# Kernel tuning notes

Measured on AMD Instinct MI355X. Metric: run time of the kernel, lower is better.

The kernel has to match this reference:

```python
import jax, jax.numpy as jnp
import numpy as np

ANCHORS = jnp.array([[1.3221, 1.73145], [3.19275, 4.00944], [5.05587, 8.09892],
                     [9.47112, 4.84053], [11.2364, 10.0071]], dtype=jnp.float32)
NUM_ANCHORS = 5
NUM_CLASSES = 20
MAX_BOXES = 50
NOOBJECT_SCALE = 1.0
OBJECT_SCALE = 5.0
COORD_SCALE = 1.0
CLASS_SCALE = 1.0
SIL_THRESH = 0.6


def iou_cwh(b1, b2):
    # boxes as (cx, cy, w, h); matches repo bbox_ious(x1y1x2y2=False)
    x1, y1, w1, h1 = b1[..., 0], b1[..., 1], b1[..., 2], b1[..., 3]
    x2, y2, w2, h2 = b2[..., 0], b2[..., 1], b2[..., 2], b2[..., 3]
    uw = jnp.maximum(x1 + w1 * 0.5, x2 + w2 * 0.5) - jnp.minimum(x1 - w1 * 0.5, x2 - w2 * 0.5)
    uh = jnp.maximum(y1 + h1 * 0.5, y2 + h2 * 0.5) - jnp.minimum(y1 - h1 * 0.5, y2 - h2 * 0.5)
    cw = w1 + w2 - uw
    ch = h1 + h2 - uh
    inter = jnp.where((cw <= 0) | (ch <= 0), 0.0, cw * ch)
    return inter / (w1 * h1 + w2 * h2 - inter)


def setup_inputs() -> dict:
    key = jax.random.key(0)
    k1, k2, k3, k4 = jax.random.split(key, 4)
    nB = 64
    output = jax.random.normal(k1, (nB, NUM_ANCHORS * (5 + NUM_CLASSES), 38, 38), dtype=jnp.float32)
    # target layout per box: (class, x, y, w, h), all normalized; x>0 marks a valid box
    cls_col = jax.random.randint(k2, (nB, MAX_BOXES, 1), 0, NUM_CLASSES).astype(jnp.float32)
    xy = jax.random.uniform(k3, (nB, MAX_BOXES, 2), minval=0.05, maxval=0.95)
    wh = jax.random.uniform(k4, (nB, MAX_BOXES, 2), minval=0.02, maxval=0.3)
    target = jnp.concatenate([cls_col, xy, wh], axis=-1).reshape(nB, MAX_BOXES * 5)
    return {"output": output, "target": target}


def region_loss(output, target):
    nB = output.shape[0]
    nA, nC = NUM_ANCHORS, NUM_CLASSES
    nH, nW = output.shape[2], output.shape[3]
    out = output.reshape(nB, nA, 5 + nC, nH, nW)
    x = jax.nn.sigmoid(out[:, :, 0])
    y = jax.nn.sigmoid(out[:, :, 1])
    w = out[:, :, 2]
    h = out[:, :, 3]
    conf = jax.nn.sigmoid(out[:, :, 4])
    # [nB,nA,nC,nH,nW] -> [nB*nA*nH*nW, nC] (matches torch transpose/view order)
    cls_logits = jnp.transpose(out[:, :, 5:], (0, 1, 3, 4, 2)).reshape(-1, nC)

    sg = jax.lax.stop_gradient
    aw, ah = ANCHORS[:, 0], ANCHORS[:, 1]
    grid_x = jnp.arange(nW, dtype=jnp.float32)[None, None, None, :]
    grid_y = jnp.arange(nH, dtype=jnp.float32)[None, None, :, None]
    px = sg(x) + grid_x
    py = sg(y) + grid_y
    pw = jnp.exp(sg(w)) * aw[None, :, None, None]
    ph = jnp.exp(sg(h)) * ah[None, :, None, None]
    pred_boxes = jnp.stack([px, py, pw, ph], axis=-1)  # [nB,nA,nH,nW,4]

    # ---- build_targets (vectorized) ----
    tgt = sg(target).reshape(nB, MAX_BOXES, 5)
    gcls = tgt[:, :, 0]
    gx = tgt[:, :, 1] * nW
    gy = tgt[:, :, 2] * nH
    gw = tgt[:, :, 3] * nW
    gh = tgt[:, :, 4] * nH
    # loop breaks at first x==0 -> cumulative validity
    valid = jnp.cumprod((tgt[:, :, 1] != 0).astype(jnp.int32), axis=1).astype(bool)

    # silence conf_mask where any-GT IoU > thresh
    pb_flat = pred_boxes.reshape(nB, nA * nH * nW, 4)
    gt_boxes = jnp.stack([gx, gy, gw, gh], axis=-1)  # [nB,50,4]
    ious = iou_cwh(pb_flat[:, :, None, :], gt_boxes[:, None, :, :])  # [nB,nAnc,50]
    ious = jnp.where(valid[:, None, :], ious, 0.0)
    max_iou = jnp.max(ious, axis=2)
    conf_mask = jnp.where(max_iou > SIL_THRESH, 0.0, NOOBJECT_SCALE).reshape(nB, nA, nH, nW)

    # seen < 12800 defaults
    shp = (nB, nA, nH, nW)
    coord_mask = jnp.ones(shp, jnp.float32)
    tx = jnp.full(shp, 0.5, jnp.float32)
    ty = jnp.full(shp, 0.5, jnp.float32)
    tw = jnp.zeros(shp, jnp.float32)
    th = jnp.zeros(shp, jnp.float32)
    tconf = jnp.zeros(shp, jnp.float32)
    tcls = jnp.zeros(shp, jnp.float32)
    cls_mask = jnp.zeros(shp, jnp.float32)

    # best anchor per GT by (0,0,w,h) IoU; argmax keeps first max like the strict '>' loop
    zA = jnp.zeros_like(aw)
    anchor_boxes = jnp.stack([zA, zA, aw, ah], axis=-1)  # [nA,4]
    zg = jnp.zeros_like(gw)
    gt_wh = jnp.stack([zg, zg, gw, gh], axis=-1)  # [nB,50,4]
    a_iou = iou_cwh(gt_wh[:, :, None, :], anchor_boxes[None, None, :, :])  # [nB,50,nA]
    best_n = jnp.argmax(a_iou, axis=2)  # [nB,50]

    gi = jnp.clip(gx.astype(jnp.int32), 0, nW - 1)
    gj = jnp.clip(gy.astype(jnp.int32), 0, nH - 1)
    aw_b = aw[best_n]
    ah_b = ah[best_n]
    tx_v = gx - gi.astype(jnp.float32)
    ty_v = gy - gj.astype(jnp.float32)
    tw_v = jnp.log(gw / aw_b)
    th_v = jnp.log(gh / ah_b)
    b_ix = jnp.arange(nB)
    pred_at = pred_boxes[b_ix[:, None], best_n, gj, gi]  # [nB,50,4]
    iou_gt = iou_cwh(gt_boxes, pred_at)  # [nB,50]

    def step(carry, t):
        cm, clm, tx_, ty_, tw_, th_, tcf, tcl = carry
        bsel = jnp.where(valid[:, t], b_ix, nB)  # out-of-bounds -> dropped
        n, j, i = best_n[:, t], gj[:, t], gi[:, t]
        st = lambda a, v: a.at[bsel, n, j, i].set(v, mode='drop')
        cm = st(cm, jnp.full((nB,), OBJECT_SCALE, jnp.float32))
        clm = st(clm, jnp.ones((nB,), jnp.float32))
        tx_ = st(tx_, tx_v[:, t])
        ty_ = st(ty_, ty_v[:, t])
        tw_ = st(tw_, tw_v[:, t])
        th_ = st(th_, th_v[:, t])
        tcf = st(tcf, iou_gt[:, t])
        tcl = st(tcl, gcls[:, t])
        return (cm, clm, tx_, ty_, tw_, th_, tcf, tcl), None

    init = (conf_mask, cls_mask, tx, ty, tw, th, tconf, tcls)
    (conf_mask, cls_mask, tx, ty, tw, th, tconf, tcls), _ = jax.lax.scan(
        step, init, jnp.arange(MAX_BOXES))

    # ---- losses ----
    cmf = jnp.sqrt(conf_mask)
    loss_x = COORD_SCALE * jnp.sum((x * coord_mask - tx * coord_mask) ** 2) / 2.0
    loss_y = COORD_SCALE * jnp.sum((y * coord_mask - ty * coord_mask) ** 2) / 2.0
    loss_w = COORD_SCALE * jnp.sum((w * coord_mask - tw * coord_mask) ** 2) / 2.0
    loss_h = COORD_SCALE * jnp.sum((h * coord_mask - th * coord_mask) ** 2) / 2.0
    loss_conf = jnp.sum((conf * cmf - tconf * cmf) ** 2) / 2.0
    logp = jax.nn.log_softmax(cls_logits, axis=-1)
    labels = tcls.reshape(-1).astype(jnp.int32)
    ce = -jnp.take_along_axis(logp, labels[:, None], axis=1)[:, 0]
    loss_cls = CLASS_SCALE * jnp.sum(ce * cls_mask.reshape(-1))
    return loss_x + loss_y + loss_w + loss_h + loss_conf + loss_cls


def reference(output, target):
    return region_loss(output, target)
```

## Files before the change

### kernel.cpp

```cpp
#include <hip/hip_runtime.h>
#include <math.h>

#define NA 5
#define NC 20
#define NH 38
#define NW 38
#define MAX_BOXES 50
#define SPAT (NH * NW)
#define CELLS_PER_B (NA * SPAT)
#define TPB 256
#define CELLS_PER_T 2
#define CPB (TPB * CELLS_PER_T)
#define GX ((CELLS_PER_B + CPB - 1) / CPB)
#define OBJECT_SCALE 5.0f
#define NOOBJECT_SCALE 1.0f

__constant__ float c_aw[NA]  = {1.3221f, 3.19275f, 5.05587f, 9.47112f, 11.2364f};
__constant__ float c_ah[NA]  = {1.73145f, 4.00944f, 8.09892f, 4.84053f, 10.0071f};
__constant__ float c_iaw[NA] = {1.f/1.3221f, 1.f/3.19275f, 1.f/5.05587f, 1.f/9.47112f, 1.f/11.2364f};
__constant__ float c_iah[NA] = {1.f/1.73145f, 1.f/4.00944f, 1.f/8.09892f, 1.f/4.84053f, 1.f/10.0071f};

__device__ __forceinline__ float fexp(float v) { return __expf(v); }
__device__ __forceinline__ float flog(float v) { return __logf(v); }
__device__ __forceinline__ float frcp(float v) { return __builtin_amdgcn_rcpf(v); }
__device__ __forceinline__ float fsig(float v) { return frcp(1.f + __expf(-v)); }

__device__ __forceinline__ float iou_fast(float x1, float y1, float w1, float h1,
                                          float x2, float y2, float w2, float h2) {
  float uw = fmaxf(x1 + w1 * 0.5f, x2 + w2 * 0.5f) - fminf(x1 - w1 * 0.5f, x2 - w2 * 0.5f);
  float uh = fmaxf(y1 + h1 * 0.5f, y2 + h2 * 0.5f) - fminf(y1 - h1 * 0.5f, y2 - h2 * 0.5f);
  float cw = w1 + w2 - uw;
  float ch = h1 + h2 - uh;
  float inter = (cw <= 0.f || ch <= 0.f) ? 0.f : cw * ch;
  return inter * frcp(w1 * h1 + w2 * h2 - inter);
}

__device__ __forceinline__ float iou_wh_exact(float w1, float h1, float w2, float h2) {
  float uw = fmaxf(w1 * 0.5f, w2 * 0.5f) - fminf(-w1 * 0.5f, -w2 * 0.5f);
  float uh = fmaxf(h1 * 0.5f, h2 * 0.5f) - fminf(-h1 * 0.5f, -h2 * 0.5f);
  float cw = w1 + w2 - uw;
  float ch = h1 + h2 - uh;
  float inter = (cw <= 0.f || ch <= 0.f) ? 0.f : cw * ch;
  return inter / (w1 * h1 + w2 * h2 - inter);
}

__global__ __launch_bounds__(TPB) void region_loss_kernel(
    const float* __restrict__ out, const float* __restrict__ target,
    float* __restrict__ partials) {
  const int b = blockIdx.y;
  const int s0 = blockIdx.x * CPB;
  const int tid = threadIdx.x;

  __shared__ float4 sb_lo[MAX_BOXES];
  __shared__ float  sb_ag[MAX_BOXES];
  __shared__ int s_wcnt;
  __shared__ int s_wcell[MAX_BOXES];
  __shared__ float s_wdata[MAX_BOXES][6];
  __shared__ float s_red[TPB / 64];

  int sC[CELLS_PER_T];
  bool ok[CELLS_PER_T];
  const float* basep[CELLS_PER_T];
  float v0[CELLS_PER_T], v1[CELLS_PER_T], v2[CELLS_PER_T], v3[CELLS_PER_T], v4[CELLS_PER_T];
  float fi[CELLS_PER_T], fj[CELLS_PER_T], paw[CELLS_PER_T], pah[CELLS_PER_T];
#pragma unroll
  for (int q = 0; q < CELLS_PER_T; ++q) {
    int s = s0 + q * TPB + tid;
    ok[q] = (s < CELLS_PER_B);
    int sc = ok[q] ? s : 0;
    sC[q] = ok[q] ? s : -1;
    unsigned a = (unsigned)sc / SPAT;
    unsigned r = (unsigned)sc - a * SPAT;
    unsigned j = r / NW, i = r - j * NW;
    fi[q] = (float)i; fj[q] = (float)j;
    paw[q] = c_aw[a]; pah[q] = c_ah[a];
    const float* bp = out + ((size_t)(b * NA + a) * 25) * SPAT + r;
    basep[q] = bp;
    v0[q] = bp[0];
    v1[q] = bp[SPAT];
    v2[q] = bp[2 * SPAT];
    v3[q] = bp[3 * SPAT];
    v4[q] = bp[4 * SPAT];
  }

  if (tid == TPB - 1) s_wcnt = 0;
  __syncthreads();

  if (tid < 64) {
    int t = tid;
    float cls = 0.f, x = 0.f, y = 0.f, w = 0.f, h = 0.f;
    if (t < MAX_BOXES) {
      const float* tg = target + (size_t)(b * MAX_BOXES + t) * 5;
      cls = tg[0]; x = tg[1]; y = tg[2]; w = tg[3]; h = tg[4];
    }
    unsigned long long nz = __ballot(t < MAX_BOXES && x != 0.f);
    unsigned long long low = (t < 63) ? ((1ull << (t + 1)) - 1ull) : ~0ull;
    bool valid = (t < MAX_BOXES) && ((nz & low) == low);

    float gx = x * NW, gy = y * NH, gw = w * NW, gh = h * NH;

    int best = 0; float bestiou = -1.f;
#pragma unroll
    for (int a2 = 0; a2 < NA; ++a2) {
      float aiou = iou_wh_exact(gw, gh, c_aw[a2], c_ah[a2]);
      if (aiou > bestiou) { bestiou = aiou; best = a2; }
    }
    int gi = min(max((int)gx, 0), NW - 1);
    int gj = min(max((int)gy, 0), NH - 1);

    const float* pb = out + ((size_t)(b * NA + best) * 25) * SPAT + gj * NW + gi;
    float px = fsig(pb[0]) + (float)gi;
    float py = fsig(pb[SPAT]) + (float)gj;
    float pw2 = fexp(pb[2 * SPAT]) * c_aw[best];
    float ph2 = fexp(pb[3 * SPAT]) * c_ah[best];
    float iou_gt = iou_fast(gx, gy, gw, gh, px, py, pw2, ph2);

    int cell = best * SPAT + gj * NW + gi;
    unsigned long long vm = __ballot(valid);
    bool winner = valid;
    for (int tp = 0; tp < MAX_BOXES; ++tp) {
      int c2 = __shfl(cell, tp);
      if (tp > t && ((vm >> tp) & 1ull) && c2 == cell) winner = false;
    }

    if (t < MAX_BOXES) {
      if (valid) {
        sb_lo[t] = make_float4(gx - gw * 0.5f, gx + gw * 0.5f,
                               gy - gh * 0.5f, gy + gh * 0.5f);
        sb_ag[t] = 0.375f * (gw * gh);
      } else {
        sb_lo[t] = make_float4(1e30f, 1e30f, 1e30f, 1e30f);
        sb_ag[t] = 0.f;
      }
      if (winner && cell >= s0 && cell < s0 + CPB) {
        int k = atomicAdd(&s_wcnt, 1);
        s_wcell[k] = cell;
        s_wdata[k][0] = gx - (float)gi;
        s_wdata[k][1] = gy - (float)gj;
        s_wdata[k][2] = flog(gw * c_iaw[best]);
        s_wdata[k][3] = flog(gh * c_iah[best]);
        s_wdata[k][4] = iou_gt;
        s_wdata[k][5] = cls;
      }
    }
  }
  __syncthreads();

  float xs[CELLS_PER_T], ys[CELLS_PER_T], cs[CELLS_PER_T];
  float plx[CELLS_PER_T], phx[CELLS_PER_T], ply[CELLS_PER_T], phy[CELLS_PER_T];
  float ap[CELLS_PER_T], msc[CELLS_PER_T];
#pragma unroll
  for (int q = 0; q < CELLS_PER_T; ++q) {
    xs[q] = fsig(v0[q]);
    ys[q] = fsig(v1[q]);
    cs[q] = fsig(v4[q]);
    float pw = fexp(v2[q]) * paw[q], ph = fexp(v3[q]) * pah[q];
    float px = xs[q] + fi[q], py = ys[q] + fj[q];
    plx[q] = px - pw * 0.5f; phx[q] = px + pw * 0.5f;
    ply[q] = py - ph * 0.5f; phy[q] = py + ph * 0.5f;
    ap[q] = 0.375f * (pw * ph);
    msc[q] = -1e30f;
  }

#pragma unroll
  for (int c0 = 0; c0 < MAX_BOXES; c0 += 10) {
    float4 bl[10]; float bag[10];
#pragma unroll
    for (int u = 0; u < 10; ++u) { bl[u] = sb_lo[c0 + u]; bag[u] = sb_ag[c0 + u]; }
#pragma unroll
    for (int u = 0; u < 10; ++u) {
#pragma unroll
      for (int q = 0; q < CELLS_PER_T; ++q) {
        float cw = fminf(phx[q], bl[u].y) - fmaxf(plx[q], bl[u].x);
        float ch = fminf(phy[q], bl[u].w) - fmaxf(ply[q], bl[u].z);
        cw = fmaxf(cw, 0.f);
        msc[q] = fmaxf(msc[q], fmaf(cw, ch, -bag[u]));
      }
    }
  }

  int cnt = s_wcnt;
  float acc = 0.f;
#pragma unroll
  for (int q = 0; q < CELLS_PER_T; ++q) {
    if (!ok[q]) continue;
    float cmask = (msc[q] > ap[q]) ? 0.f : NOOBJECT_SCALE;
    float tx = 0.5f, ty = 0.5f, tw = 0.f, th = 0.f, tconf = 0.f, clsloss = 0.f;
    for (int k = 0; k < cnt; ++k) {
      if (s_wcell[k] == sC[q]) {
        cmask = OBJECT_SCALE;
        tx = s_wdata[k][0]; ty = s_wdata[k][1];
        tw = s_wdata[k][2]; th = s_wdata[k][3];
        tconf = s_wdata[k][4];
        int label = (int)s_wdata[k][5];
        const float* cb = basep[q] + 5 * SPAT;
        float m = -1e30f, lv = 0.f;
        for (int c = 0; c < NC; ++c) {
          float vv = cb[c * SPAT];
          if (c == label) lv = vv;
          m = fmaxf(m, vv);
        }
        float ssum = 0.f;
        for (int c = 0; c < NC; ++c) ssum += fexp(cb[c * SPAT] - m);
        clsloss = (m + flog(ssum)) - lv;
      }
    }
    float dx = xs[q] - tx, dy = ys[q] - ty, dw = v2[q] - tw, dh = v3[q] - th;
    float dc = cs[q] - tconf;
    acc += 0.5f * (dx * dx + dy * dy + dw * dw + dh * dh + cmask * (dc * dc)) + clsloss;
  }

  for (int o = 32; o > 0; o >>= 1) acc += __shfl_down(acc, o, 64);
  int wid = tid >> 6, lane = tid & 63;
  if (lane == 0) s_red[wid] = acc;
  __syncthreads();
  if (tid == 0) {
    float v = 0.f;
#pragma unroll
    for (int wdx = 0; wdx < TPB / 64; ++wdx) v += s_red[wdx];
    partials[blockIdx.y * GX + blockIdx.x] = v;
  }
}

__global__ __launch_bounds__(256) void reduce_kernel(
    const float* __restrict__ partials, int n, float* __restrict__ outv) {
  float acc = 0.f;
  for (int i = threadIdx.x; i < n; i += 256) acc += partials[i];
  for (int o = 32; o > 0; o >>= 1) acc += __shfl_down(acc, o, 64);
  __shared__ float s_red[4];
  int wid = threadIdx.x >> 6, lane = threadIdx.x & 63;
  if (lane == 0) s_red[wid] = acc;
  __syncthreads();
  if (threadIdx.x == 0) outv[0] = s_red[0] + s_red[1] + s_red[2] + s_red[3];
}

extern "C" void kernel_launch(void* const* d_in, const int* in_sizes, int n_in,
                              void* d_out, int out_size, void* d_ws, size_t ws_size,
                              hipStream_t stream) {
  const float* out = (const float*)d_in[0];
  const float* target = (const float*)d_in[1];
  int nB = in_sizes[0] / (NA * (5 + NC) * SPAT);
  float* partials = (float*)d_ws;
  hipLaunchKernelGGL(region_loss_kernel, dim3(GX, nB), dim3(TPB), 0, stream,
                     out, target, partials);
  hipLaunchKernelGGL(reduce_kernel, dim3(1), dim3(256), 0, stream,
                     partials, GX * nB, (float*)d_out);
}
```

Before: 118.4 us.

## Split winner-cell correction into prep kernel and simplify main loss pass

Moves the per-target processing (anchor matching, winner detection, box prep) into a separate per-batch prep kernel. That kernel writes the box list and a per-batch correction delta, the object-cell loss minus the default no-object loss. The main kernel then computes only the uniform default loss per cell, dropping the per-cell scan over winners, the softmax branch and the per-block target recomputation. The cost is an extra launch and global round trip for the boxes, and it relies on the winner cell's default term being subtracted exactly.

Result: faster. 104.7 us (-11.5%).

```diff
diff --git a/kernel.cpp b/kernel.cpp
--- a/kernel.cpp
+++ b/kernel.cpp
@@ -44,8 +44,108 @@
   return inter / (w1 * h1 + w2 * h2 - inter);
 }
 
-__global__ __launch_bounds__(TPB) void region_loss_kernel(
+__global__ __launch_bounds__(64) void prep_kernel(
     const float* __restrict__ out, const float* __restrict__ target,
+    float4* __restrict__ boxes, float* __restrict__ delta) {
+  const int b = blockIdx.x;
+  const int t = threadIdx.x;
+  __shared__ float4 sb_lo[MAX_BOXES];
+  __shared__ float  sb_ag[MAX_BOXES];
+
+  float cls = 0.f, x = 0.f, y = 0.f, w = 0.f, h = 0.f;
+  if (t < MAX_BOXES) {
+    const float* tg = target + (size_t)(b * MAX_BOXES + t) * 5;
+    cls = tg[0]; x = tg[1]; y = tg[2]; w = tg[3]; h = tg[4];
+  }
+  unsigned long long nz = __ballot(t < MAX_BOXES && x != 0.f);
+  unsigned long long low = (t < 63) ? ((1ull << (t + 1)) - 1ull) : ~0ull;
+  bool valid = (t < MAX_BOXES) && ((nz & low) == low);
+
+  float gx = x * NW, gy = y * NH, gw = w * NW, gh = h * NH;
+
+  int best = 0; float bestiou = -1.f;
+#pragma unroll
+  for (int a2 = 0; a2 < NA; ++a2) {
+    float aiou = iou_wh_exact(gw, gh, c_aw[a2], c_ah[a2]);
+    if (aiou > bestiou) { bestiou = aiou; best = a2; }
+  }
+  int gi = min(max((int)gx, 0), NW - 1);
+  int gj = min(max((int)gy, 0), NH - 1);
+  int cell = best * SPAT + gj * NW + gi;
+
+  unsigned long long vm = __ballot(valid);
+  bool winner = valid;
+  for (int tp = 0; tp < MAX_BOXES; ++tp) {
+    int c2 = __shfl(cell, tp);
+    if (tp > t && ((vm >> tp) & 1ull) && c2 == cell) winner = false;
+  }
+
+  float4 lo; float ag;
+  if (valid) {
+    lo = make_float4(gx - gw * 0.5f, gx + gw * 0.5f, gy - gh * 0.5f, gy + gh * 0.5f);
+    ag = 0.375f * (gw * gh);
+  } else {
+    lo = make_float4(1e30f, 1e30f, 1e30f, 1e30f);
+    ag = 0.f;
+  }
+  if (t < MAX_BOXES) {
+    boxes[(size_t)(b * MAX_BOXES + t) * 2]     = lo;
+    boxes[(size_t)(b * MAX_BOXES + t) * 2 + 1] = make_float4(ag, 0.f, 0.f, 0.f);
+    sb_lo[t] = lo;
+    sb_ag[t] = ag;
+  }
+  __syncthreads();
+
+  float d = 0.f;
+  if (winner) {
+    const float* bp = out + ((size_t)(b * NA + best) * 25) * SPAT + gj * NW + gi;
+    float v0 = bp[0], v1 = bp[SPAT], v2 = bp[2 * SPAT], v3 = bp[3 * SPAT], v4 = bp[4 * SPAT];
+    float xs = fsig(v0), ys = fsig(v1), cs = fsig(v4);
+    float pw = fexp(v2) * c_aw[best], ph = fexp(v3) * c_ah[best];
+    float px = xs + (float)gi, py = ys + (float)gj;
+    float plx = px - pw * 0.5f, phx = px + pw * 0.5f;
+    float ply = py - ph * 0.5f, phy = py + ph * 0.5f;
+    float ap = 0.375f * (pw * ph);
+
+    float msc = -1e30f;
+    for (int t2 = 0; t2 < MAX_BOXES; ++t2) {
+      float4 l2 = sb_lo[t2];
+      float cw = fminf(phx, l2.y) - fmaxf(plx, l2.x);
+      float ch = fminf(phy, l2.w) - fmaxf(ply, l2.z);
+      cw = fmaxf(cw, 0.f);
+      msc = fmaxf(msc, fmaf(cw, ch, -sb_ag[t2]));
+    }
+    float cmask_def = (msc > ap) ? 0.f : NOOBJECT_SCALE;
+    float xd = xs - 0.5f, yd = ys - 0.5f;
+    float D = 0.5f * (xd * xd + yd * yd + v2 * v2 + v3 * v3 + cmask_def * (cs * cs));
+
+    float txv = gx - (float)gi, tyv = gy - (float)gj;
+    float twv = flog(gw * c_iaw[best]), thv = flog(gh * c_iah[best]);
+    float tconf = iou_fast(gx, gy, gw, gh, px, py, pw, ph);
+    float dx = xs - txv, dy = ys - tyv, dwv = v2 - twv, dhv = v3 - thv, dc = cs - tconf;
+
+    int label = (int)cls;
+    const float* cb = bp + 5 * SPAT;
+    float m = -1e30f, lv = 0.f;
+    for (int c = 0; c < NC; ++c) {
+      float vv = cb[c * SPAT];
+      if (c == label) lv = vv;
+      m = fmaxf(m, vv);
+    }
+    float ssum = 0.f;
+    for (int c = 0; c < NC; ++c) ssum += fexp(cb[c * SPAT] - m);
+    float ce = (m + flog(ssum)) - lv;
+
+    float W = 0.5f * (dx * dx + dy * dy + dwv * dwv + dhv * dhv +
+                      OBJECT_SCALE * (dc * dc)) + ce;
+    d = W - D;
+  }
+  for (int o = 32; o > 0; o >>= 1) d += __shfl_down(d, o, 64);
+  if (t == 0) delta[b] = d;
+}
+
+__global__ __launch_bounds__(TPB) void main_kernel(
+    const float* __restrict__ out, const float4* __restrict__ boxes,
     float* __restrict__ partials) {
   const int b = blockIdx.y;
   const int s0 = blockIdx.x * CPB;
@@ -53,14 +153,17 @@
 
   __shared__ float4 sb_lo[MAX_BOXES];
   __shared__ float  sb_ag[MAX_BOXES];
-  __shared__ int s_wcnt;
-  __shared__ int s_wcell[MAX_BOXES];
-  __shared__ float s_wdata[MAX_BOXES][6];
-  __shared__ float s_red[TPB / 64];
-
-  int sC[CELLS_PER_T];
+  __shared__ float  s_red[TPB / 64];
+
+  if (tid < MAX_BOXES) {
+    float4 lo = boxes[(size_t)(b * MAX_BOXES + tid) * 2];
+    float4 hi = boxes[(size_t)(b * MAX_BOXES + tid) * 2 + 1];
+    sb_lo[tid] = lo;
+    sb_ag[tid] = hi.x;
+  }
+  __syncthreads();
+
   bool ok[CELLS_PER_T];
-  const float* basep[CELLS_PER_T];
   float v0[CELLS_PER_T], v1[CELLS_PER_T], v2[CELLS_PER_T], v3[CELLS_PER_T], v4[CELLS_PER_T];
   float fi[CELLS_PER_T], fj[CELLS_PER_T], paw[CELLS_PER_T], pah[CELLS_PER_T];
 #pragma unroll
@@ -68,83 +171,18 @@
     int s = s0 + q * TPB + tid;
     ok[q] = (s < CELLS_PER_B);
     int sc = ok[q] ? s : 0;
-    sC[q] = ok[q] ? s : -1;
     unsigned a = (unsigned)sc / SPAT;
     unsigned r = (unsigned)sc - a * SPAT;
     unsigned j = r / NW, i = r - j * NW;
     fi[q] = (float)i; fj[q] = (float)j;
     paw[q] = c_aw[a]; pah[q] = c_ah[a];
     const float* bp = out + ((size_t)(b * NA + a) * 25) * SPAT + r;
-    basep[q] = bp;
     v0[q] = bp[0];
     v1[q] = bp[SPAT];
     v2[q] = bp[2 * SPAT];
     v3[q] = bp[3 * SPAT];
     v4[q] = bp[4 * SPAT];
   }
-
-  if (tid == TPB - 1) s_wcnt = 0;
-  __syncthreads();
-
-  if (tid < 64) {
-    int t = tid;
-    float cls = 0.f, x = 0.f, y = 0.f, w = 0.f, h = 0.f;
-    if (t < MAX_BOXES) {
-      const float* tg = target + (size_t)(b * MAX_BOXES + t) * 5;
-      cls = tg[0]; x = tg[1]; y = tg[2]; w = tg[3]; h = tg[4];
-    }
-    unsigned long long nz = __ballot(t < MAX_BOXES && x != 0.f);
-    unsigned long long low = (t < 63) ? ((1ull << (t + 1)) - 1ull) : ~0ull;
-    bool valid = (t < MAX_BOXES) && ((nz & low) == low);
-
-    float gx = x * NW, gy = y * NH, gw = w * NW, gh = h * NH;
-
-    int best = 0; float bestiou = -1.f;
-#pragma unroll
-    for (int a2 = 0; a2 < NA; ++a2) {
-      float aiou = iou_wh_exact(gw, gh, c_aw[a2], c_ah[a2]);
-      if (aiou > bestiou) { bestiou = aiou; best = a2; }
-    }
-    int gi = min(max((int)gx, 0), NW - 1);
-    int gj = min(max((int)gy, 0), NH - 1);
-
-    const float* pb = out + ((size_t)(b * NA + best) * 25) * SPAT + gj * NW + gi;
-    float px = fsig(pb[0]) + (float)gi;
-    float py = fsig(pb[SPAT]) + (float)gj;
-    float pw2 = fexp(pb[2 * SPAT]) * c_aw[best];
-    float ph2 = fexp(pb[3 * SPAT]) * c_ah[best];
-    float iou_gt = iou_fast(gx, gy, gw, gh, px, py, pw2, ph2);
-
-    int cell = best * SPAT + gj * NW + gi;
-    unsigned long long vm = __ballot(valid);
-    bool winner = valid;
-    for (int tp = 0; tp < MAX_BOXES; ++tp) {
-      int c2 = __shfl(cell, tp);
-      if (tp > t && ((vm >> tp) & 1ull) && c2 == cell) winner = false;
-    }
-
-    if (t < MAX_BOXES) {
-      if (valid) {
-        sb_lo[t] = make_float4(gx - gw * 0.5f, gx + gw * 0.5f,
-                               gy - gh * 0.5f, gy + gh * 0.5f);
-        sb_ag[t] = 0.375f * (gw * gh);
-      } else {
-        sb_lo[t] = make_float4(1e30f, 1e30f, 1e30f, 1e30f);
-        sb_ag[t] = 0.f;
-      }
-      if (winner && cell >= s0 && cell < s0 + CPB) {
-        int k = atomicAdd(&s_wcnt, 1);
-        s_wcell[k] = cell;
-        s_wdata[k][0] = gx - (float)gi;
-        s_wdata[k][1] = gy - (float)gj;
-        s_wdata[k][2] = flog(gw * c_iaw[best]);
-        s_wdata[k][3] = flog(gh * c_iah[best]);
-        s_wdata[k][4] = iou_gt;
-        s_wdata[k][5] = cls;
-      }
-    }
-  }
-  __syncthreads();
 
   float xs[CELLS_PER_T], ys[CELLS_PER_T], cs[CELLS_PER_T];
   float plx[CELLS_PER_T], phx[CELLS_PER_T], ply[CELLS_PER_T], phy[CELLS_PER_T];
@@ -179,35 +217,14 @@
     }
   }
 
-  int cnt = s_wcnt;
   float acc = 0.f;
 #pragma unroll
   for (int q = 0; q < CELLS_PER_T; ++q) {
     if (!ok[q]) continue;
     float cmask = (msc[q] > ap[q]) ? 0.f : NOOBJECT_SCALE;
-    float tx = 0.5f, ty = 0.5f, tw = 0.f, th = 0.f, tconf = 0.f, clsloss = 0.f;
-    for (int k = 0; k < cnt; ++k) {
-      if (s_wcell[k] == sC[q]) {
-        cmask = OBJECT_SCALE;
-        tx = s_wdata[k][0]; ty = s_wdata[k][1];
-        tw = s_wdata[k][2]; th = s_wdata[k][3];
-        tconf = s_wdata[k][4];
-        int label = (int)s_wdata[k][5];
-        const float* cb = basep[q] + 5 * SPAT;
-        float m = -1e30f, lv = 0.f;
-        for (int c = 0; c < NC; ++c) {
-          float vv = cb[c * SPAT];
-          if (c == label) lv = vv;
-          m = fmaxf(m, vv);
-        }
-        float ssum = 0.f;
-        for (int c = 0; c < NC; ++c) ssum += fexp(cb[c * SPAT] - m);
-        clsloss = (m + flog(ssum)) - lv;
-      }
-    }
-    float dx = xs[q] - tx, dy = ys[q] - ty, dw = v2[q] - tw, dh = v3[q] - th;
-    float dc = cs[q] - tconf;
-    acc += 0.5f * (dx * dx + dy * dy + dw * dw + dh * dh + cmask * (dc * dc)) + clsloss;
+    float xd = xs[q] - 0.5f, yd = ys[q] - 0.5f;
+    acc += 0.5f * (xd * xd + yd * yd + v2[q] * v2[q] + v3[q] * v3[q] +
+                   cmask * (cs[q] * cs[q]));
   }
 
   for (int o = 32; o > 0; o >>= 1) acc += __shfl_down(acc, o, 64);
@@ -223,9 +240,9 @@
 }
 
 __global__ __launch_bounds__(256) void reduce_kernel(
-    const float* __restrict__ partials, int n, float* __restrict__ outv) {
+    const float* __restrict__ vals, int n, float* __restrict__ outv) {
   float acc = 0.f;
-  for (int i = threadIdx.x; i < n; i += 256) acc += partials[i];
+  for (int i = threadIdx.x; i < n; i += 256) acc += vals[i];
   for (int o = 32; o > 0; o >>= 1) acc += __shfl_down(acc, o, 64);
   __shared__ float s_red[4];
   int wid = threadIdx.x >> 6, lane = threadIdx.x & 63;
@@ -240,9 +257,15 @@
   const float* out = (const float*)d_in[0];
   const float* target = (const float*)d_in[1];
   int nB = in_sizes[0] / (NA * (5 + NC) * SPAT);
-  float* partials = (float*)d_ws;
-  hipLaunchKernelGGL(region_loss_kernel, dim3(GX, nB), dim3(TPB), 0, stream,
-                     out, target, partials);
+
+  float4* boxes = (float4*)d_ws;
+  float* partials = (float*)((char*)d_ws + (size_t)nB * MAX_BOXES * 2 * sizeof(float4));
+  float* delta = partials + GX * nB;
+
+  hipLaunchKernelGGL(prep_kernel, dim3(nB), dim3(64), 0, stream,
+                     out, target, boxes, delta);
+  hipLaunchKernelGGL(main_kernel, dim3(GX, nB), dim3(TPB), 0, stream,
+                     out, boxes, partials);
   hipLaunchKernelGGL(reduce_kernel, dim3(1), dim3(256), 0, stream,
-                     partials, GX * nB, (float*)d_out);
-}
+                     partials, GX * nB + nB, (float*)d_out);
+}
```
